# Kernel optimization log

Hardware: AMD Instinct MI355X
Metric: run time of the kernel (lower is better)

Reference implementation:

```python
import jax, jax.numpy as jnp
import numpy as np

N = 100000
E = 1600000
IN_C = 256
HID = 256
OUT_C = 10
G = 64  # number of graphs in batch


def setup_inputs() -> dict:
    key = jax.random.key(0)
    k1, k2, k3, k4, k5, k6, k7 = jax.random.split(key, 7)
    x = jax.random.normal(k1, (N, IN_C), dtype=jnp.float32)
    edge_index = jax.random.randint(k2, (2, E), 0, N, dtype=jnp.int64)
    batch = jnp.sort(jax.random.randint(k3, (N,), 0, G, dtype=jnp.int64))
    # GCNConv weight (glorot-ish) and bias
    W1 = jax.random.normal(k4, (IN_C, HID), dtype=jnp.float32) / np.sqrt(IN_C)
    b1 = jnp.zeros((HID,), dtype=jnp.float32)
    # final Linear
    W2 = jax.random.normal(k5, (HID, OUT_C), dtype=jnp.float32) / np.sqrt(HID)
    b2 = jax.random.normal(k6, (OUT_C,), dtype=jnp.float32) * 0.01
    return {"x": x, "edge_index": edge_index, "batch": batch,
            "W1": W1, "b1": b1, "W2": W2, "b2": b2}


def reference(x, edge_index, batch, W1, b1, W2, b2):
    # ---- GCNConv(in_channels, hidden_dim), add_self_loops=True, symmetric norm ----
    src = edge_index[0]
    dst = edge_index[1]
    loop = jnp.arange(N, dtype=src.dtype)
    src = jnp.concatenate([src, loop])  # [E+N]
    dst = jnp.concatenate([dst, loop])
    # degree on destination nodes (incl. self-loops) -> >= 1 everywhere
    deg = jax.ops.segment_sum(jnp.ones_like(dst, dtype=x.dtype), dst, num_segments=N)
    dinv = jax.lax.rsqrt(deg)  # deg >= 1, safe
    h = x @ W1  # linear transform first (PyG GCNConv order)
    norm = dinv[src] * dinv[dst]  # [E+N]
    msgs = h[src] * norm[:, None]  # gather + scale
    agg = jax.ops.segment_sum(msgs, dst, num_segments=N) + b1  # scatter-add + bias
    # ---- relu; dropout is identity in eval mode ----
    hrelu = jax.nn.relu(agg)
    # ---- global_mean_pool over batch ids ----
    sums = jax.ops.segment_sum(hrelu, batch, num_segments=G)
    counts = jax.ops.segment_sum(jnp.ones((N,), dtype=x.dtype), batch, num_segments=G)
    pooled = sums / jnp.maximum(counts, 1.0)[:, None]  # [G, HID]
    # ---- final linear ----
    return pooled @ W2 + b2
```

## Files before the change

### kernel.cpp

```cpp
#include <hip/hip_runtime.h>

#define NN 100000
#define EE 1600000
#define C 256
#define OUTC 10
#define NG 64

#define NBK 391
#define CHUNK 16384
#define NBLK1 ((EE + CHUNK - 1) / CHUNK)

#define NODES_PER_GROUP 8
#define NODES_PER_BLOCK 32

typedef __bf16 bf16x8 __attribute__((ext_vector_type(8)));
typedef float f32x4 __attribute__((ext_vector_type(4)));
typedef float f32x2 __attribute__((ext_vector_type(2)));

__device__ __forceinline__ ushort f2bf(float f) {
    unsigned u = __float_as_uint(f);
    return (ushort)((u + 0x7fffu + ((u >> 16) & 1u)) >> 16);
}
__device__ __forceinline__ bf16x8 as_bf16x8(uint4 v) {
    union { uint4 u; bf16x8 b; } c; c.u = v; return c.b;
}

__device__ __forceinline__ uchar f2fp8(float f) {
    return (uchar)(__builtin_amdgcn_cvt_pk_fp8_f32(f, 0.f, 0, false) & 0xff);
}
__device__ __forceinline__ void acc_fp8x4(float4& s, unsigned v) {
    f32x2 lo = __builtin_amdgcn_cvt_pk_f32_fp8(v, false);
    f32x2 hi = __builtin_amdgcn_cvt_pk_f32_fp8(v, true);
    s.x += lo[0]; s.y += lo[1]; s.z += hi[0]; s.w += hi[1];
}

__global__ __launch_bounds__(1024) void count_kernel(const int* __restrict__ batch,
                                                     float* __restrict__ cnt) {
    __shared__ int h[NG];
    if (threadIdx.x < NG) h[threadIdx.x] = 0;
    __syncthreads();
    int i = blockIdx.x * blockDim.x + threadIdx.x;
    if (i < NN) atomicAdd(&h[batch[i]], 1);
    __syncthreads();
    if (threadIdx.x < NG) {
        int v = h[threadIdx.x];
        if (v > 0) atomicAdd(&cnt[threadIdx.x], (float)v);
    }
}

__global__ __launch_bounds__(256) void bucket_hist_kernel(const int* __restrict__ ei,
                                                          int* __restrict__ bhist) {
    __shared__ int h[NBK];
    for (int t = threadIdx.x; t < NBK; t += 256) h[t] = 0;
    __syncthreads();
    const int base = blockIdx.x * CHUNK;
    const int end = min(base + CHUNK, EE);
    for (int e = base + threadIdx.x; e < end; e += 256)
        atomicAdd(&h[ei[EE + e] >> 8], 1);
    __syncthreads();
    for (int t = threadIdx.x; t < NBK; t += 256)
        if (h[t]) atomicAdd(&bhist[t], h[t]);
}

__global__ void bucket_scan_kernel(const int* __restrict__ bhist,
                                   int* __restrict__ bbase, int* __restrict__ bcur) {
    if (threadIdx.x == 0) {
        int acc = 0;
        for (int i = 0; i < NBK; i++) {
            bbase[i] = acc; bcur[i] = acc; acc += bhist[i];
        }
        bbase[NBK] = acc;
    }
}

__global__ __launch_bounds__(256) void bucket_scatter_kernel(const int* __restrict__ ei,
                                                             int* __restrict__ bcur,
                                                             unsigned* __restrict__ bmaj) {
    __shared__ int h[NBK];
    for (int t = threadIdx.x; t < NBK; t += 256) h[t] = 0;
    __syncthreads();
    const int base = blockIdx.x * CHUNK;
    const int end = min(base + CHUNK, EE);
    for (int e = base + threadIdx.x; e < end; e += 256)
        atomicAdd(&h[ei[EE + e] >> 8], 1);
    __syncthreads();
    for (int t = threadIdx.x; t < NBK; t += 256) {
        int c = h[t];
        h[t] = c ? atomicAdd(&bcur[t], c) : 0;
    }
    __syncthreads();
    for (int e = base + threadIdx.x; e < end; e += 256) {
        int d = ei[EE + e];
        int s = ei[e];
        int b = d >> 8;
        int p = atomicAdd(&h[b], 1);
        bmaj[p] = (unsigned)s | ((unsigned)(d & 255) << 17);
    }
}

__global__ __launch_bounds__(256) void bucket_csr_kernel(const unsigned* __restrict__ bmaj,
                                                         const int* __restrict__ bbase,
                                                         int* __restrict__ rowend,
                                                         float* __restrict__ dinv,
                                                         int* __restrict__ csrcol) {
    __shared__ int h[256];
    __shared__ int sc[256];
    __shared__ int cur[256];
    const int b = blockIdx.x;
    const int t = threadIdx.x;
    const int e0 = bbase[b], e1 = bbase[b + 1];
    h[t] = 0;
    __syncthreads();
    for (int e = e0 + t; e < e1; e += 256)
        atomicAdd(&h[bmaj[e] >> 17], 1);
    __syncthreads();
    int deg = h[t];
    sc[t] = deg;
    __syncthreads();
    for (int off = 1; off < 256; off <<= 1) {
        int tmp = (t >= off) ? sc[t - off] : 0;
        __syncthreads();
        sc[t] += tmp;
        __syncthreads();
    }
    int incl = sc[t];
    int node = b * 256 + t;
    if (node < NN) {
        rowend[node] = e0 + incl;
        dinv[node] = rsqrtf((float)deg + 1.0f);
    }
    cur[t] = e0 + incl - deg;
    __syncthreads();
    for (int e = e0 + t; e < e1; e += 256) {
        unsigned v = bmaj[e];
        int p = atomicAdd(&cur[v >> 17], 1);
        csrcol[p] = (int)(v & 0x1FFFFu);
    }
}

__global__ __launch_bounds__(256) void w1pack_kernel(const float* __restrict__ W1,
                                                     ushort* __restrict__ w1f) {
    int t = blockIdx.x * 256 + threadIdx.x;
    int k = t >> 8, n = t & 255;
    int kb = k >> 5, q = (k >> 3) & 3, j = k & 7;
    int nt = n >> 4, ln = (n & 15) + q * 16;
    w1f[(size_t)(((kb * 16 + nt) * 64) + ln) * 8 + j] = f2bf(W1[t]);
}

__global__ __launch_bounds__(256) void gemm_mfma_kernel(const float* __restrict__ x,
                                                        const ushort* __restrict__ w1f,
                                                        const float* __restrict__ dinv,
                                                        uchar* __restrict__ g) {
    const int lane = threadIdx.x & 63;
    const int wid = threadIdx.x >> 6;
    const int wave = blockIdx.x * 4 + wid;
    const int r0 = wave * 32;
    if (r0 >= NN) return;
    const int mrow = lane & 15;
    const int q = lane >> 4;

    f32x4 acc[2][16];
    #pragma unroll
    for (int mt = 0; mt < 2; mt++)
        #pragma unroll
        for (int nt = 0; nt < 16; nt++)
            acc[mt][nt] = (f32x4){0.f, 0.f, 0.f, 0.f};

    const float* xp0 = x + (size_t)(r0 + mrow) * C + q * 8;
    const float* xp1 = xp0 + (size_t)16 * C;
    const ushort* bp = w1f + (size_t)lane * 8;

    #pragma unroll 1
    for (int kb = 0; kb < 8; kb++) {
        const int ko = kb * 32;
        float4 a0lo = *(const float4*)(xp0 + ko);
        float4 a0hi = *(const float4*)(xp0 + ko + 4);
        float4 a1lo = *(const float4*)(xp1 + ko);
        float4 a1hi = *(const float4*)(xp1 + ko + 4);
        bf16x8 a0, a1;
        a0[0] = (__bf16)a0lo.x; a0[1] = (__bf16)a0lo.y;
        a0[2] = (__bf16)a0lo.z; a0[3] = (__bf16)a0lo.w;
        a0[4] = (__bf16)a0hi.x; a0[5] = (__bf16)a0hi.y;
        a0[6] = (__bf16)a0hi.z; a0[7] = (__bf16)a0hi.w;
        a1[0] = (__bf16)a1lo.x; a1[1] = (__bf16)a1lo.y;
        a1[2] = (__bf16)a1lo.z; a1[3] = (__bf16)a1lo.w;
        a1[4] = (__bf16)a1hi.x; a1[5] = (__bf16)a1hi.y;
        a1[6] = (__bf16)a1hi.z; a1[7] = (__bf16)a1hi.w;

        const ushort* bkb = bp + (size_t)kb * 16 * 512;
        #pragma unroll
        for (int nt = 0; nt < 16; nt++) {
            bf16x8 bb = as_bf16x8(*(const uint4*)(bkb + (size_t)nt * 512));
            acc[0][nt] = __builtin_amdgcn_mfma_f32_16x16x32_bf16(a0, bb, acc[0][nt], 0, 0, 0);
            acc[1][nt] = __builtin_amdgcn_mfma_f32_16x16x32_bf16(a1, bb, acc[1][nt], 0, 0, 0);
        }
    }

    #pragma unroll
    for (int mt = 0; mt < 2; mt++) {
        #pragma unroll
        for (int r = 0; r < 4; r++) {
            int row = r0 + mt * 16 + q * 4 + r;
            float dv = dinv[row];
            uchar* gp = g + (size_t)row * C + mrow;
            #pragma unroll
            for (int nt = 0; nt < 16; nt++)
                gp[nt * 16] = f2fp8(acc[mt][nt][r] * dv);
        }
    }
}

__global__ __launch_bounds__(256) void agg_pool_kernel(const unsigned* __restrict__ g32,
                                                       const int* __restrict__ rowend,
                                                       const int* __restrict__ csrcol,
                                                       const float* __restrict__ dinv,
                                                       const float* __restrict__ b1,
                                                       const int* __restrict__ batch,
                                                       float* __restrict__ sums) {
    const int lane = threadIdx.x & 63;
    const int wid = threadIdx.x >> 6;
    const int c4 = lane * 4;
    const int nodeA = blockIdx.x * NODES_PER_BLOCK + wid * NODES_PER_GROUP;
    const float4 bv = *(const float4*)&b1[c4];

    float4 pool = make_float4(0.f, 0.f, 0.f, 0.f);
    int curb = -1;
    int rprev = (nodeA == 0) ? 0 : rowend[nodeA - 1];

    #pragma unroll 1
    for (int i = nodeA; i < nodeA + NODES_PER_GROUP; i++) {
        int r1 = rowend[i];
        int r0 = rprev;
        rprev = r1;
        int bi = batch[i];
        if (bi != curb) {
            if (curb >= 0) {
                atomicAdd(&sums[curb * C + c4 + 0], pool.x);
                atomicAdd(&sums[curb * C + c4 + 1], pool.y);
                atomicAdd(&sums[curb * C + c4 + 2], pool.z);
                atomicAdd(&sums[curb * C + c4 + 3], pool.w);
            }
            curb = bi;
            pool = make_float4(0.f, 0.f, 0.f, 0.f);
        }
        float4 s = make_float4(0.f, 0.f, 0.f, 0.f);
        acc_fp8x4(s, g32[(size_t)i * 64 + lane]);
        int e = r0;
        for (; e + 8 <= r1; e += 8) {
            int i0 = csrcol[e],     i1 = csrcol[e + 1];
            int i2 = csrcol[e + 2], i3 = csrcol[e + 3];
            int i4 = csrcol[e + 4], i5 = csrcol[e + 5];
            int i6 = csrcol[e + 6], i7 = csrcol[e + 7];
            unsigned v0 = g32[(size_t)i0 * 64 + lane];
            unsigned v1 = g32[(size_t)i1 * 64 + lane];
            unsigned v2 = g32[(size_t)i2 * 64 + lane];
            unsigned v3 = g32[(size_t)i3 * 64 + lane];
            unsigned v4 = g32[(size_t)i4 * 64 + lane];
            unsigned v5 = g32[(size_t)i5 * 64 + lane];
            unsigned v6 = g32[(size_t)i6 * 64 + lane];
            unsigned v7 = g32[(size_t)i7 * 64 + lane];
            acc_fp8x4(s, v0); acc_fp8x4(s, v1); acc_fp8x4(s, v2); acc_fp8x4(s, v3);
            acc_fp8x4(s, v4); acc_fp8x4(s, v5); acc_fp8x4(s, v6); acc_fp8x4(s, v7);
        }
        for (; e < r1; e++)
            acc_fp8x4(s, g32[(size_t)csrcol[e] * 64 + lane]);

        float dv = dinv[i];
        pool.x += fmaxf(fmaf(dv, s.x, bv.x), 0.f);
        pool.y += fmaxf(fmaf(dv, s.y, bv.y), 0.f);
        pool.z += fmaxf(fmaf(dv, s.z, bv.z), 0.f);
        pool.w += fmaxf(fmaf(dv, s.w, bv.w), 0.f);
    }
    if (curb >= 0) {
        atomicAdd(&sums[curb * C + c4 + 0], pool.x);
        atomicAdd(&sums[curb * C + c4 + 1], pool.y);
        atomicAdd(&sums[curb * C + c4 + 2], pool.z);
        atomicAdd(&sums[curb * C + c4 + 3], pool.w);
    }
}

__global__ __launch_bounds__(256) void final_kernel(const float* __restrict__ sums,
                                                    const float* __restrict__ cnt,
                                                    const float* __restrict__ W2,
                                                    const float* __restrict__ b2,
                                                    float* __restrict__ out) {
    __shared__ float p[C];
    int gi = blockIdx.x;
    float cdiv = fmaxf(cnt[gi], 1.0f);
    p[threadIdx.x] = sums[gi * C + threadIdx.x] / cdiv;
    __syncthreads();
    if (threadIdx.x < OUTC) {
        float acc = b2[threadIdx.x];
        for (int k = 0; k < C; k++) acc += p[k] * W2[k * OUTC + threadIdx.x];
        out[gi * OUTC + threadIdx.x] = acc;
    }
}

extern "C" void kernel_launch(void* const* d_in, const int* in_sizes, int n_in,
                              void* d_out, int out_size, void* d_ws, size_t ws_size,
                              hipStream_t stream) {
    const float* x     = (const float*)d_in[0];
    const int*   ei    = (const int*)d_in[1];
    const int*   batch = (const int*)d_in[2];
    const float* W1    = (const float*)d_in[3];
    const float* b1    = (const float*)d_in[4];
    const float* W2    = (const float*)d_in[5];
    const float* b2    = (const float*)d_in[6];
    float* out = (float*)d_out;

    char* w = (char*)d_ws;
    size_t off = 0;
    auto carve = [&](size_t bytes) {
        void* p = w + off;
        off = (off + bytes + 255) & ~(size_t)255;
        return p;
    };
    uchar*    g        = (uchar*)   carve((size_t)NN * C);
    int*      rowend   = (int*)     carve((size_t)NN * 4);
    float*    dinv     = (float*)   carve((size_t)NN * 4);
    int*      csrcol   = (int*)     carve((size_t)EE * 4);
    unsigned* bmaj     = (unsigned*)carve((size_t)EE * 4);
    int*      bbase    = (int*)     carve((size_t)(NBK + 1) * 4);
    int*      bcur     = (int*)     carve((size_t)NBK * 4);
    ushort*   w1f      = (ushort*)  carve((size_t)C * C * 2);
    int*      bhist    = (int*)     carve((size_t)NBK * 4);
    float*    sums     = (float*)   carve((size_t)NG * C * 4);
    float*    cnt      = (float*)   carve((size_t)NG * 4);
    size_t zero_bytes = (size_t)((char*)cnt + (size_t)NG * 4 - (char*)bhist);

    hipMemsetAsync(bhist, 0, zero_bytes, stream);

    bucket_hist_kernel<<<NBLK1, 256, 0, stream>>>(ei, bhist);
    bucket_scan_kernel<<<1, 64, 0, stream>>>(bhist, bbase, bcur);
    bucket_scatter_kernel<<<NBLK1, 256, 0, stream>>>(ei, bcur, bmaj);
    bucket_csr_kernel<<<NBK, 256, 0, stream>>>(bmaj, bbase, rowend, dinv, csrcol);
    count_kernel<<<(NN + 1023) / 1024, 1024, 0, stream>>>(batch, cnt);
    w1pack_kernel<<<C * C / 256, 256, 0, stream>>>(W1, w1f);
    gemm_mfma_kernel<<<(NN / 32 + 3) / 4, 256, 0, stream>>>(x, w1f, dinv, g);
    agg_pool_kernel<<<NN / NODES_PER_BLOCK, 256, 0, stream>>>(
        (const unsigned*)g, rowend, csrcol, dinv, b1, batch, sums);
    final_kernel<<<NG, 256, 0, stream>>>(sums, cnt, W2, b2, out);
}
```

Measured before the change: 432.9 us.

## Slice CSR by source-node range across 16-node groups for gather locality

Builds a source-sliced CSR in which each group of 16 destination nodes has its edges ordered by 13 source-id slices. The aggregation kernel then walks the slices in order for all 16 nodes at once, so concurrent waves gather from similar regions of the fp8 feature table and get better L2 reuse. Edge indices are loaded cooperatively per wave and broadcast with readlane. The single-thread bucket scan is also replaced by a parallel block scan. In exchange, the per-group edge loop is serial with data-dependent while loops, each wave holds 16 float4 accumulators, and the CSR build does more shared-memory work.

```diff
diff --git a/kernel.cpp b/kernel.cpp
--- a/kernel.cpp
+++ b/kernel.cpp
@@ -10,8 +10,11 @@
 #define CHUNK 16384
 #define NBLK1 ((EE + CHUNK - 1) / CHUNK)
 
-#define NODES_PER_GROUP 8
-#define NODES_PER_BLOCK 32
+#define NSL 13
+#define SLSH 13
+#define GPW 16
+#define NGRP (NN / GPW)
+#define GPB (256 / GPW)
 
 typedef __bf16 bf16x8 __attribute__((ext_vector_type(8)));
 typedef float f32x4 __attribute__((ext_vector_type(4)));
@@ -62,15 +65,23 @@
         if (h[t]) atomicAdd(&bhist[t], h[t]);
 }
 
-__global__ void bucket_scan_kernel(const int* __restrict__ bhist,
-                                   int* __restrict__ bbase, int* __restrict__ bcur) {
-    if (threadIdx.x == 0) {
-        int acc = 0;
-        for (int i = 0; i < NBK; i++) {
-            bbase[i] = acc; bcur[i] = acc; acc += bhist[i];
-        }
-        bbase[NBK] = acc;
-    }
+__global__ __launch_bounds__(512) void bucket_scan_kernel(const int* __restrict__ bhist,
+                                                          int* __restrict__ bbase,
+                                                          int* __restrict__ bcur) {
+    __shared__ int sc[512];
+    const int t = threadIdx.x;
+    int v = (t < NBK) ? bhist[t] : 0;
+    sc[t] = v;
+    __syncthreads();
+    for (int off = 1; off < 512; off <<= 1) {
+        int tmp = (t >= off) ? sc[t - off] : 0;
+        __syncthreads();
+        sc[t] += tmp;
+        __syncthreads();
+    }
+    int excl = sc[t] - v;
+    if (t < NBK) { bbase[t] = excl; bcur[t] = excl; }
+    if (t == 0) bbase[NBK] = sc[511];
 }
 
 __global__ __launch_bounds__(256) void bucket_scatter_kernel(const int* __restrict__ ei,
@@ -100,41 +111,79 @@
 
 __global__ __launch_bounds__(256) void bucket_csr_kernel(const unsigned* __restrict__ bmaj,
                                                          const int* __restrict__ bbase,
-                                                         int* __restrict__ rowend,
+                                                         int* __restrict__ E,
                                                          float* __restrict__ dinv,
-                                                         int* __restrict__ csrcol) {
-    __shared__ int h[256];
-    __shared__ int sc[256];
-    __shared__ int cur[256];
+                                                         int* __restrict__ csr2) {
+    __shared__ int h[256][NSL];
+    __shared__ int cur[256][NSL];
+    __shared__ int cgs[GPB][NSL];
+    __shared__ int segb[GPB][NSL];
+    __shared__ int gbase[GPB];
     const int b = blockIdx.x;
     const int t = threadIdx.x;
     const int e0 = bbase[b], e1 = bbase[b + 1];
-    h[t] = 0;
-    __syncthreads();
-    for (int e = e0 + t; e < e1; e += 256)
-        atomicAdd(&h[bmaj[e] >> 17], 1);
-    __syncthreads();
-    int deg = h[t];
-    sc[t] = deg;
-    __syncthreads();
-    for (int off = 1; off < 256; off <<= 1) {
-        int tmp = (t >= off) ? sc[t - off] : 0;
-        __syncthreads();
-        sc[t] += tmp;
-        __syncthreads();
-    }
-    int incl = sc[t];
-    int node = b * 256 + t;
-    if (node < NN) {
-        rowend[node] = e0 + incl;
-        dinv[node] = rsqrtf((float)deg + 1.0f);
-    }
-    cur[t] = e0 + incl - deg;
+    const int node0 = b * 256;
+    const int nvalid = min(256, NN - node0);
+    const int ngv = nvalid >> 4;
+
+    #pragma unroll
+    for (int s = 0; s < NSL; s++) h[t][s] = 0;
     __syncthreads();
     for (int e = e0 + t; e < e1; e += 256) {
         unsigned v = bmaj[e];
-        int p = atomicAdd(&cur[v >> 17], 1);
-        csrcol[p] = (int)(v & 0x1FFFFu);
+        atomicAdd(&h[v >> 17][(v & 0x1FFFFu) >> SLSH], 1);
+    }
+    __syncthreads();
+    if (t < nvalid) {
+        int deg = 0;
+        #pragma unroll
+        for (int s = 0; s < NSL; s++) deg += h[t][s];
+        dinv[node0 + t] = rsqrtf((float)deg + 1.0f);
+    }
+    for (int idx = t; idx < ngv * NSL; idx += 256) {
+        int g = idx / NSL, s = idx % NSL;
+        int c = 0;
+        #pragma unroll
+        for (int n = 0; n < GPW; n++) c += h[g * GPW + n][s];
+        cgs[g][s] = c;
+    }
+    __syncthreads();
+    if (t == 0) {
+        int acc = e0;
+        for (int g = 0; g < ngv; g++) {
+            gbase[g] = acc;
+            for (int s = 0; s < NSL; s++) acc += cgs[g][s];
+        }
+    }
+    __syncthreads();
+    if (t < ngv) {
+        int run = gbase[t];
+        for (int s = 0; s < NSL; s++) { segb[t][s] = run; run += cgs[t][s]; }
+    }
+    __syncthreads();
+    for (int idx = t; idx < ngv * NSL; idx += 256) {
+        int g = idx / NSL, s = idx % NSL;
+        int run = segb[g][s];
+        #pragma unroll
+        for (int n = 0; n < GPW; n++) {
+            int nn = g * GPW + n;
+            cur[nn][s] = run;
+            run += h[nn][s];
+        }
+    }
+    __syncthreads();
+    const int grpG0 = b * GPB;
+    for (int idx = t; idx < nvalid * NSL; idx += 256) {
+        int nl = idx / NSL, s = idx % NSL;
+        int g = nl >> 4, n = nl & 15;
+        E[(((size_t)(grpG0 + g)) * NSL + s) * GPW + n] = cur[nl][s] + h[nl][s];
+    }
+    __syncthreads();
+    for (int e = e0 + t; e < e1; e += 256) {
+        unsigned v = bmaj[e];
+        int src = (int)(v & 0x1FFFFu);
+        int p = atomicAdd(&cur[v >> 17][src >> SLSH], 1);
+        csr2[p] = src;
     }
 }
 
@@ -211,27 +260,58 @@
 }
 
 __global__ __launch_bounds__(256) void agg_pool_kernel(const unsigned* __restrict__ g32,
-                                                       const int* __restrict__ rowend,
-                                                       const int* __restrict__ csrcol,
+                                                       const int* __restrict__ E,
+                                                       const int* __restrict__ csr2,
                                                        const float* __restrict__ dinv,
                                                        const float* __restrict__ b1,
                                                        const int* __restrict__ batch,
                                                        float* __restrict__ sums) {
     const int lane = threadIdx.x & 63;
     const int wid = threadIdx.x >> 6;
+    const int grp = blockIdx.x * 4 + wid;
+    if (grp >= NGRP) return;
     const int c4 = lane * 4;
-    const int nodeA = blockIdx.x * NODES_PER_BLOCK + wid * NODES_PER_GROUP;
+    const int node0 = grp * GPW;
+
+    float4 acc[GPW];
+    #pragma unroll
+    for (int n = 0; n < GPW; n++) acc[n] = make_float4(0.f, 0.f, 0.f, 0.f);
+
+    int p = (grp == 0) ? 0 : E[(((size_t)(grp - 1)) * NSL + (NSL - 1)) * GPW + (GPW - 1)];
+
+    #pragma unroll 1
+    for (int s = 0; s < NSL; s++) {
+        int eb[GPW];
+        const int* Ep = E + (((size_t)grp) * NSL + s) * GPW;
+        *(int4*)&eb[0]  = *(const int4*)(Ep + 0);
+        *(int4*)&eb[4]  = *(const int4*)(Ep + 4);
+        *(int4*)&eb[8]  = *(const int4*)(Ep + 8);
+        *(int4*)&eb[12] = *(const int4*)(Ep + 12);
+        const int segbase = p;
+        const int cnt = eb[GPW - 1] - segbase;
+        #pragma unroll 1
+        for (int kb = 0; kb < cnt; kb += 64) {
+            int rec = 0;
+            if (kb + lane < cnt) rec = csr2[segbase + kb + lane];
+            const int chunk_end = segbase + min(kb + 64, cnt);
+            #pragma unroll
+            for (int n = 0; n < GPW; n++) {
+                int lim = min(eb[n], chunk_end);
+                while (p < lim) {
+                    int idx = __builtin_amdgcn_readlane(rec, p - segbase - kb);
+                    acc_fp8x4(acc[n], g32[(size_t)idx * 64 + lane]);
+                    p++;
+                }
+            }
+        }
+    }
+
     const float4 bv = *(const float4*)&b1[c4];
-
     float4 pool = make_float4(0.f, 0.f, 0.f, 0.f);
     int curb = -1;
-    int rprev = (nodeA == 0) ? 0 : rowend[nodeA - 1];
-
-    #pragma unroll 1
-    for (int i = nodeA; i < nodeA + NODES_PER_GROUP; i++) {
-        int r1 = rowend[i];
-        int r0 = rprev;
-        rprev = r1;
+    #pragma unroll
+    for (int n = 0; n < GPW; n++) {
+        int i = node0 + n;
         int bi = batch[i];
         if (bi != curb) {
             if (curb >= 0) {
@@ -243,33 +323,13 @@
             curb = bi;
             pool = make_float4(0.f, 0.f, 0.f, 0.f);
         }
-        float4 s = make_float4(0.f, 0.f, 0.f, 0.f);
-        acc_fp8x4(s, g32[(size_t)i * 64 + lane]);
-        int e = r0;
-        for (; e + 8 <= r1; e += 8) {
-            int i0 = csrcol[e],     i1 = csrcol[e + 1];
-            int i2 = csrcol[e + 2], i3 = csrcol[e + 3];
-            int i4 = csrcol[e + 4], i5 = csrcol[e + 5];
-            int i6 = csrcol[e + 6], i7 = csrcol[e + 7];
-            unsigned v0 = g32[(size_t)i0 * 64 + lane];
-            unsigned v1 = g32[(size_t)i1 * 64 + lane];
-            unsigned v2 = g32[(size_t)i2 * 64 + lane];
-            unsigned v3 = g32[(size_t)i3 * 64 + lane];
-            unsigned v4 = g32[(size_t)i4 * 64 + lane];
-            unsigned v5 = g32[(size_t)i5 * 64 + lane];
-            unsigned v6 = g32[(size_t)i6 * 64 + lane];
-            unsigned v7 = g32[(size_t)i7 * 64 + lane];
-            acc_fp8x4(s, v0); acc_fp8x4(s, v1); acc_fp8x4(s, v2); acc_fp8x4(s, v3);
-            acc_fp8x4(s, v4); acc_fp8x4(s, v5); acc_fp8x4(s, v6); acc_fp8x4(s, v7);
-        }
-        for (; e < r1; e++)
-            acc_fp8x4(s, g32[(size_t)csrcol[e] * 64 + lane]);
-
+        float4 sv = acc[n];
+        acc_fp8x4(sv, g32[(size_t)i * 64 + lane]);
         float dv = dinv[i];
-        pool.x += fmaxf(fmaf(dv, s.x, bv.x), 0.f);
-        pool.y += fmaxf(fmaf(dv, s.y, bv.y), 0.f);
-        pool.z += fmaxf(fmaf(dv, s.z, bv.z), 0.f);
-        pool.w += fmaxf(fmaf(dv, s.w, bv.w), 0.f);
+        pool.x += fmaxf(fmaf(dv, sv.x, bv.x), 0.f);
+        pool.y += fmaxf(fmaf(dv, sv.y, bv.y), 0.f);
+        pool.z += fmaxf(fmaf(dv, sv.z, bv.z), 0.f);
+        pool.w += fmaxf(fmaf(dv, sv.w, bv.w), 0.f);
     }
     if (curb >= 0) {
         atomicAdd(&sums[curb * C + c4 + 0], pool.x);
@@ -316,10 +376,10 @@
         return p;
     };
     uchar*    g        = (uchar*)   carve((size_t)NN * C);
-    int*      rowend   = (int*)     carve((size_t)NN * 4);
     float*    dinv     = (float*)   carve((size_t)NN * 4);
-    int*      csrcol   = (int*)     carve((size_t)EE * 4);
+    int*      csr2     = (int*)     carve((size_t)EE * 4);
     unsigned* bmaj     = (unsigned*)carve((size_t)EE * 4);
+    int*      Earr     = (int*)     carve((size_t)NGRP * NSL * GPW * 4);
     int*      bbase    = (int*)     carve((size_t)(NBK + 1) * 4);
     int*      bcur     = (int*)     carve((size_t)NBK * 4);
     ushort*   w1f      = (ushort*)  carve((size_t)C * C * 2);
@@ -331,13 +391,13 @@
     hipMemsetAsync(bhist, 0, zero_bytes, stream);
 
     bucket_hist_kernel<<<NBLK1, 256, 0, stream>>>(ei, bhist);
-    bucket_scan_kernel<<<1, 64, 0, stream>>>(bhist, bbase, bcur);
+    bucket_scan_kernel<<<1, 512, 0, stream>>>(bhist, bbase, bcur);
     bucket_scatter_kernel<<<NBLK1, 256, 0, stream>>>(ei, bcur, bmaj);
-    bucket_csr_kernel<<<NBK, 256, 0, stream>>>(bmaj, bbase, rowend, dinv, csrcol);
+    bucket_csr_kernel<<<NBK, 256, 0, stream>>>(bmaj, bbase, Earr, dinv, csr2);
     count_kernel<<<(NN + 1023) / 1024, 1024, 0, stream>>>(batch, cnt);
     w1pack_kernel<<<C * C / 256, 256, 0, stream>>>(W1, w1f);
     gemm_mfma_kernel<<<(NN / 32 + 3) / 4, 256, 0, stream>>>(x, w1f, dinv, g);
-    agg_pool_kernel<<<NN / NODES_PER_BLOCK, 256, 0, stream>>>(
-        (const unsigned*)g, rowend, csrcol, dinv, b1, batch, sums);
+    agg_pool_kernel<<<(NGRP + 3) / 4, 256, 0, stream>>>(
+        (const unsigned*)g, Earr, csr2, dinv, b1, batch, sums);
     final_kernel<<<NG, 256, 0, stream>>>(sums, cnt, W2, b2, out);
 }
```

Result: slower. 521.9 us (+20.6%).

## Pad CSR rows to multiples of eight with a zero dummy node, parallelize bucket scan

Applied to the files above, without the earlier changes.

Each CSR row is padded to a multiple of 8 entries that point to an extra all-zero row of g (index NN), with per-bucket slack in csrcol. This lets the aggregation loop run only the unrolled 8-wide gather path and drops the scalar tail loop, which removes divergent remainder iterations. The single-thread bucket scan also becomes a 512-thread shared-memory scan. In exchange, padded rows gather extra dummy rows and csrcol uses more memory.

```diff
diff --git a/kernel.cpp b/kernel.cpp
--- a/kernel.cpp
+++ b/kernel.cpp
@@ -9,6 +9,7 @@
 #define NBK 391
 #define CHUNK 16384
 #define NBLK1 ((EE + CHUNK - 1) / CHUNK)
+#define PADSLACK 2048
 
 #define NODES_PER_GROUP 8
 #define NODES_PER_BLOCK 32
@@ -62,15 +63,23 @@
         if (h[t]) atomicAdd(&bhist[t], h[t]);
 }
 
-__global__ void bucket_scan_kernel(const int* __restrict__ bhist,
-                                   int* __restrict__ bbase, int* __restrict__ bcur) {
-    if (threadIdx.x == 0) {
-        int acc = 0;
-        for (int i = 0; i < NBK; i++) {
-            bbase[i] = acc; bcur[i] = acc; acc += bhist[i];
-        }
-        bbase[NBK] = acc;
-    }
+__global__ __launch_bounds__(512) void bucket_scan_kernel(const int* __restrict__ bhist,
+                                                          int* __restrict__ bbase,
+                                                          int* __restrict__ bcur) {
+    __shared__ int sc[512];
+    const int t = threadIdx.x;
+    int v = (t < NBK) ? bhist[t] : 0;
+    sc[t] = v;
+    __syncthreads();
+    for (int off = 1; off < 512; off <<= 1) {
+        int tmp = (t >= off) ? sc[t - off] : 0;
+        __syncthreads();
+        sc[t] += tmp;
+        __syncthreads();
+    }
+    int excl = sc[t] - v;
+    if (t < NBK) { bbase[t] = excl; bcur[t] = excl; }
+    if (t == 0) bbase[NBK] = sc[511];
 }
 
 __global__ __launch_bounds__(256) void bucket_scatter_kernel(const int* __restrict__ ei,
@@ -109,13 +118,15 @@
     const int b = blockIdx.x;
     const int t = threadIdx.x;
     const int e0 = bbase[b], e1 = bbase[b + 1];
+    const int region0 = e0 + b * PADSLACK;
     h[t] = 0;
     __syncthreads();
     for (int e = e0 + t; e < e1; e += 256)
         atomicAdd(&h[bmaj[e] >> 17], 1);
     __syncthreads();
     int deg = h[t];
-    sc[t] = deg;
+    int pd = (deg + 7) & ~7;
+    sc[t] = pd;
     __syncthreads();
     for (int off = 1; off < 256; off <<= 1) {
         int tmp = (t >= off) ? sc[t - off] : 0;
@@ -123,13 +134,14 @@
         sc[t] += tmp;
         __syncthreads();
     }
-    int incl = sc[t];
+    int pstart = region0 + sc[t] - pd;
     int node = b * 256 + t;
     if (node < NN) {
-        rowend[node] = e0 + incl;
+        rowend[node] = pstart + pd;
         dinv[node] = rsqrtf((float)deg + 1.0f);
-    }
-    cur[t] = e0 + incl - deg;
+        for (int j = deg; j < pd; j++) csrcol[pstart + j] = NN;
+    }
+    cur[t] = pstart;
     __syncthreads();
     for (int e = e0 + t; e < e1; e += 256) {
         unsigned v = bmaj[e];
@@ -139,8 +151,10 @@
 }
 
 __global__ __launch_bounds__(256) void w1pack_kernel(const float* __restrict__ W1,
-                                                     ushort* __restrict__ w1f) {
+                                                     ushort* __restrict__ w1f,
+                                                     unsigned* __restrict__ gz) {
     int t = blockIdx.x * 256 + threadIdx.x;
+    if (blockIdx.x == 0 && threadIdx.x < 64) gz[threadIdx.x] = 0;
     int k = t >> 8, n = t & 255;
     int kb = k >> 5, q = (k >> 3) & 3, j = k & 7;
     int nt = n >> 4, ln = (n & 15) + q * 16;
@@ -213,6 +227,7 @@
 __global__ __launch_bounds__(256) void agg_pool_kernel(const unsigned* __restrict__ g32,
                                                        const int* __restrict__ rowend,
                                                        const int* __restrict__ csrcol,
+                                                       const int* __restrict__ bbase,
                                                        const float* __restrict__ dinv,
                                                        const float* __restrict__ b1,
                                                        const int* __restrict__ batch,
@@ -223,10 +238,16 @@
     const int nodeA = blockIdx.x * NODES_PER_BLOCK + wid * NODES_PER_GROUP;
     const float4 bv = *(const float4*)&b1[c4];
 
+    int rprev;
+    if ((nodeA & 255) == 0) {
+        int b = nodeA >> 8;
+        rprev = bbase[b] + b * PADSLACK;
+    } else {
+        rprev = rowend[nodeA - 1];
+    }
+
     float4 pool = make_float4(0.f, 0.f, 0.f, 0.f);
     int curb = -1;
-    int rprev = (nodeA == 0) ? 0 : rowend[nodeA - 1];
-
     #pragma unroll 1
     for (int i = nodeA; i < nodeA + NODES_PER_GROUP; i++) {
         int r1 = rowend[i];
@@ -245,8 +266,8 @@
         }
         float4 s = make_float4(0.f, 0.f, 0.f, 0.f);
         acc_fp8x4(s, g32[(size_t)i * 64 + lane]);
-        int e = r0;
-        for (; e + 8 <= r1; e += 8) {
+        #pragma unroll 1
+        for (int e = r0; e < r1; e += 8) {
             int i0 = csrcol[e],     i1 = csrcol[e + 1];
             int i2 = csrcol[e + 2], i3 = csrcol[e + 3];
             int i4 = csrcol[e + 4], i5 = csrcol[e + 5];
@@ -262,9 +283,6 @@
             acc_fp8x4(s, v0); acc_fp8x4(s, v1); acc_fp8x4(s, v2); acc_fp8x4(s, v3);
             acc_fp8x4(s, v4); acc_fp8x4(s, v5); acc_fp8x4(s, v6); acc_fp8x4(s, v7);
         }
-        for (; e < r1; e++)
-            acc_fp8x4(s, g32[(size_t)csrcol[e] * 64 + lane]);
-
         float dv = dinv[i];
         pool.x += fmaxf(fmaf(dv, s.x, bv.x), 0.f);
         pool.y += fmaxf(fmaf(dv, s.y, bv.y), 0.f);
@@ -315,10 +333,10 @@
         off = (off + bytes + 255) & ~(size_t)255;
         return p;
     };
-    uchar*    g        = (uchar*)   carve((size_t)NN * C);
+    uchar*    g        = (uchar*)   carve((size_t)(NN + 1) * C);
     int*      rowend   = (int*)     carve((size_t)NN * 4);
     float*    dinv     = (float*)   carve((size_t)NN * 4);
-    int*      csrcol   = (int*)     carve((size_t)EE * 4);
+    int*      csrcol   = (int*)     carve((size_t)(EE + NBK * PADSLACK) * 4);
     unsigned* bmaj     = (unsigned*)carve((size_t)EE * 4);
     int*      bbase    = (int*)     carve((size_t)(NBK + 1) * 4);
     int*      bcur     = (int*)     carve((size_t)NBK * 4);
@@ -331,13 +349,13 @@
     hipMemsetAsync(bhist, 0, zero_bytes, stream);
 
     bucket_hist_kernel<<<NBLK1, 256, 0, stream>>>(ei, bhist);
-    bucket_scan_kernel<<<1, 64, 0, stream>>>(bhist, bbase, bcur);
+    bucket_scan_kernel<<<1, 512, 0, stream>>>(bhist, bbase, bcur);
     bucket_scatter_kernel<<<NBLK1, 256, 0, stream>>>(ei, bcur, bmaj);
     bucket_csr_kernel<<<NBK, 256, 0, stream>>>(bmaj, bbase, rowend, dinv, csrcol);
     count_kernel<<<(NN + 1023) / 1024, 1024, 0, stream>>>(batch, cnt);
-    w1pack_kernel<<<C * C / 256, 256, 0, stream>>>(W1, w1f);
+    w1pack_kernel<<<C * C / 256, 256, 0, stream>>>(W1, w1f, (unsigned*)(g + (size_t)NN * C));
     gemm_mfma_kernel<<<(NN / 32 + 3) / 4, 256, 0, stream>>>(x, w1f, dinv, g);
     agg_pool_kernel<<<NN / NODES_PER_BLOCK, 256, 0, stream>>>(
-        (const unsigned*)g, rowend, csrcol, dinv, b1, batch, sums);
+        (const unsigned*)g, rowend, csrcol, bbase, dinv, b1, batch, sums);
     final_kernel<<<NG, 256, 0, stream>>>(sums, cnt, W2, b2, out);
 }
```

Measured after the change: 424.0 us. -2.1%, faster.
